# Kernel optimization log

Measured on AMD Instinct MI355X. Metric: run time of the kernel, lower is better.

Reference implementation:

```python
import jax, jax.numpy as jnp
import numpy as np

VOCAB, EMBED, HIDDEN, NCLS = 50257, 1024, 4096, 3
B, S = 4096, 128


def ternary_quant(w):
    # Per-tensor ternary quantization: scale = mean |w|, weights in {-s, 0, +s}.
    s = jnp.mean(jnp.abs(w))
    return jnp.round(jnp.clip(w / s, -1.0, 1.0)) * s


def layer_norm(x, g, b, eps=1e-5):
    mu = jnp.mean(x, axis=-1, keepdims=True)
    var = jnp.mean(jnp.square(x - mu), axis=-1, keepdims=True)
    return (x - mu) * jax.lax.rsqrt(var + eps) * g + b


def setup_inputs() -> dict:
    key = jax.random.key(0)
    ks = jax.random.split(key, 12)
    input_ids = jax.random.randint(ks[0], (B, S), 0, VOCAB, dtype=jnp.int32)
    emb = jax.random.normal(ks[1], (VOCAB, EMBED), dtype=jnp.float32) * 0.02
    emb = emb.at[0].set(0.0)  # padding_idx=0
    w1 = jax.random.normal(ks[2], (HIDDEN, EMBED), dtype=jnp.float32) * 0.02
    b1 = jnp.zeros((HIDDEN,), jnp.float32)
    w2 = jax.random.normal(ks[3], (HIDDEN // 2, HIDDEN), dtype=jnp.float32) * 0.02
    b2 = jnp.zeros((HIDDEN // 2,), jnp.float32)
    w3 = jax.random.normal(ks[4], (NCLS, HIDDEN // 2), dtype=jnp.float32) * 0.02
    b3 = jnp.zeros((NCLS,), jnp.float32)
    g1 = jnp.ones((HIDDEN,), jnp.float32)
    beta1 = jnp.zeros((HIDDEN,), jnp.float32)
    g2 = jnp.ones((HIDDEN // 2,), jnp.float32)
    beta2 = jnp.zeros((HIDDEN // 2,), jnp.float32)
    return dict(input_ids=input_ids, emb=emb, w1=w1, b1=b1, w2=w2, b2=b2,
                w3=w3, b3=b3, g1=g1, beta1=beta1, g2=g2, beta2=beta2)


def reference(input_ids, emb, w1, b1, w2, b2, w3, b3, g1, beta1, g2, beta2):
    x = emb[input_ids]                                   # (B, S, E)
    mask = (input_ids != 0).astype(x.dtype)[..., None]   # (B, S, 1)
    x = jnp.sum(x * mask, axis=1) / jnp.clip(jnp.sum(mask, axis=1), 1.0)  # (B, E)
    h = jax.nn.gelu(layer_norm(x @ ternary_quant(w1).T + b1, g1, beta1), approximate=False)
    h = jax.nn.gelu(layer_norm(h @ ternary_quant(w2).T + b2, g2, beta2), approximate=False)
    logits = h @ ternary_quant(w3).T + b3                # (B, 3)
    return logits
```

## Files before the change

### kernel.cpp

```cpp
#include <hip/hip_runtime.h>
#include <cstdint>
#include <cstddef>


#define GAS __attribute__((address_space(1)))
#define LAS __attribute__((address_space(3)))

typedef __bf16 bf16x8 __attribute__((ext_vector_type(8)));
typedef float  f32x4  __attribute__((ext_vector_type(4)));
typedef unsigned short u16x8 __attribute__((ext_vector_type(8)));

__device__ __forceinline__ unsigned short f2bf(float f) {
    unsigned int u = __float_as_uint(f);
    u += 0x7FFFu + ((u >> 16) & 1u);
    return (unsigned short)(u >> 16);
}
__device__ __forceinline__ float bf2f(unsigned short h) {
    return __uint_as_float(((unsigned int)h) << 16);
}

static constexpr int BB = 4096;
static constexpr int SS = 128;
static constexpr int EE = 1024;
static constexpr int HH = 4096;
static constexpr int H2D = 2048;
static constexpr int VOCAB = 50257;

static constexpr size_t OFF_S    = 0;
static constexpr size_t OFF_X    = 4096;
static constexpr size_t SZ_X     = (size_t)BB * EE * 2;
static constexpr size_t OFF_EMBH = OFF_X + SZ_X;
static constexpr size_t SZ_EMBH  = (size_t)VOCAB * EE * 2;
static constexpr size_t OFF_Q1   = OFF_EMBH;
static constexpr size_t OFF_Q2   = OFF_Q1 + (size_t)HH * EE * 2;
static constexpr size_t OFF_C    = OFF_Q2 + (size_t)H2D * HH * 2;
static constexpr size_t OFF_H1   = OFF_EMBH + SZ_EMBH;
static constexpr size_t OFF_H2   = OFF_Q1;


__global__ void zero_sums(double* s) {
    if (threadIdx.x < 3) s[threadIdx.x] = 0.0;
}

__global__ __launch_bounds__(256) void emb2bf_kernel(const float* __restrict__ e,
                                                     unsigned short* __restrict__ o) {
    const int n8 = (VOCAB * EE) / 8;
    for (int i = blockIdx.x * 256 + threadIdx.x; i < n8; i += gridDim.x * 256) {
        const float4 v0 = ((const float4*)e)[2 * i];
        const float4 v1 = ((const float4*)e)[2 * i + 1];
        union { unsigned short u[8]; uint4 q; } r;
        r.u[0] = f2bf(v0.x); r.u[1] = f2bf(v0.y); r.u[2] = f2bf(v0.z); r.u[3] = f2bf(v0.w);
        r.u[4] = f2bf(v1.x); r.u[5] = f2bf(v1.y); r.u[6] = f2bf(v1.z); r.u[7] = f2bf(v1.w);
        ((uint4*)o)[i] = r.q;
    }
}

__global__ __launch_bounds__(256) void absum_all(const float* __restrict__ w1,
                                                 const float* __restrict__ w2,
                                                 const float* __restrict__ w3,
                                                 double* __restrict__ sums) {
    const int bid = blockIdx.x;
    const float* w; int n; double* out; int b0; int nb;
    if (bid < 1024)      { w = w1; n = HH * EE;  out = sums + 0; b0 = bid;        nb = 1024; }
    else if (bid < 3072) { w = w2; n = H2D * HH; out = sums + 1; b0 = bid - 1024; nb = 2048; }
    else                 { w = w3; n = 3 * H2D;  out = sums + 2; b0 = bid - 3072; nb = 24;   }
    const int tid = threadIdx.x;
    const int lane = tid & 63, wid = tid >> 6;
    double acc = 0.0;
    for (int i = b0 * 256 + tid; i < n; i += nb * 256)
        acc += (double)fabsf(w[i]);
    for (int o = 32; o; o >>= 1) acc += __shfl_down(acc, o);
    __shared__ double r[4];
    if (lane == 0) r[wid] = acc;
    __syncthreads();
    if (tid == 0) atomicAdd(out, r[0] + r[1] + r[2] + r[3]);
}

__global__ __launch_bounds__(256) void quant_all(const float* __restrict__ w1,
                                                 const float* __restrict__ w2,
                                                 const double* __restrict__ sums,
                                                 unsigned short* __restrict__ q1,
                                                 unsigned short* __restrict__ q2) {
    const int bid = blockIdx.x;
    const float* w; int n; unsigned short* q; int b0; int nb; double ssum; double dn;
    if (bid < 4096) { w = w1; n = HH * EE;  q = q1; b0 = bid;        nb = 4096; ssum = sums[0]; dn = (double)(HH) * EE; }
    else            { w = w2; n = H2D * HH; q = q2; b0 = bid - 4096; nb = 8192; ssum = sums[1]; dn = (double)(H2D) * HH; }
    const float inv_s = (float)(dn / ssum);
    for (int i = b0 * 256 + threadIdx.x; i < n; i += nb * 256) {
        float t = w[i] * inv_s;
        t = fminf(1.f, fmaxf(-1.f, t));
        q[i] = f2bf(rintf(t));
    }
}

__global__ __launch_bounds__(256) void pool_kernel(const int* __restrict__ ids,
                                                   const unsigned short* __restrict__ embh,
                                                   unsigned short* __restrict__ X) {
    const int tid  = threadIdx.x;
    const int half = tid >> 7;
    const int t    = tid & 127;
    const int b    = blockIdx.x * 2 + half;
    __shared__ int sid[2 * SS];
    sid[tid] = ids[(size_t)blockIdx.x * 2 * SS + tid];
    __syncthreads();
    const int col  = t * 8;
    const int base = half * SS;
    float a[8] = {};
    int cnt = 0;
    #pragma unroll 8
    for (int s = 0; s < SS; ++s) {
        const int id = sid[base + s];
        cnt += (id != 0);
        const u16x8 v = *(const u16x8*)(embh + (size_t)id * EE + col);
        #pragma unroll
        for (int j = 0; j < 8; ++j) a[j] += bf2f(v[j]);
    }
    const float inv = 1.f / (float)(cnt ? cnt : 1);
    u16x8 o;
    #pragma unroll
    for (int j = 0; j < 8; ++j) o[j] = f2bf(a[j] * inv);
    *(u16x8*)(X + (size_t)b * EE + col) = o;
}

__global__ __launch_bounds__(256) void gemm_bt(const unsigned short* __restrict__ A,
                                               const unsigned short* __restrict__ B,
                                               float* __restrict__ C, int M, int N, int K) {
    __shared__ unsigned short sA[128 * 32];
    __shared__ unsigned short sB[128 * 32];
    const int tid  = threadIdx.x;
    const int wid  = tid >> 6;
    const int lane = tid & 63;
    const int wm = wid >> 1, wn = wid & 1;
    const int quad = lane >> 4;
    const int l16  = lane & 15;
    const int mBase = blockIdx.y * 128;
    const int nBase = blockIdx.x * 128;

    f32x4 acc[4][4] = {};

    const int srow = tid >> 2;
    const int scol = (tid & 3) * 8;
    const size_t aOff0 = (size_t)(mBase + srow) * K + scol;
    const size_t aOff1 = aOff0 + (size_t)64 * K;
    const size_t bOff0 = (size_t)(nBase + srow) * K + scol;
    const size_t bOff1 = bOff0 + (size_t)64 * K;
    unsigned short* ldsA0 = &sA[wid * 512];
    unsigned short* ldsA1 = &sA[2048 + wid * 512];
    unsigned short* ldsB0 = &sB[wid * 512];
    unsigned short* ldsB1 = &sB[2048 + wid * 512];

    for (int k0 = 0; k0 < K; k0 += 32) {
        __syncthreads();
        __builtin_amdgcn_global_load_lds((const GAS void*)(A + aOff0 + k0), (LAS void*)ldsA0, 16, 0, 0);
        __builtin_amdgcn_global_load_lds((const GAS void*)(A + aOff1 + k0), (LAS void*)ldsA1, 16, 0, 0);
        __builtin_amdgcn_global_load_lds((const GAS void*)(B + bOff0 + k0), (LAS void*)ldsB0, 16, 0, 0);
        __builtin_amdgcn_global_load_lds((const GAS void*)(B + bOff1 + k0), (LAS void*)ldsB1, 16, 0, 0);
        __syncthreads();

        bf16x8 af[4], bfr[4];
        #pragma unroll
        for (int i = 0; i < 4; ++i) {
            const int rowA = wm * 64 + i * 16 + l16;
            af[i]  = *(const bf16x8*)(&sA[rowA * 32 + quad * 8]);
            const int rowB = wn * 64 + i * 16 + l16;
            bfr[i] = *(const bf16x8*)(&sB[rowB * 32 + quad * 8]);
        }
        #pragma unroll
        for (int i = 0; i < 4; ++i)
            #pragma unroll
            for (int j = 0; j < 4; ++j)
                acc[i][j] = __builtin_amdgcn_mfma_f32_16x16x32_bf16(af[i], bfr[j], acc[i][j], 0, 0, 0);
    }

    #pragma unroll
    for (int i = 0; i < 4; ++i) {
        const int row0 = mBase + wm * 64 + i * 16 + quad * 4;
        #pragma unroll
        for (int j = 0; j < 4; ++j) {
            const int col = nBase + wn * 64 + j * 16 + l16;
            #pragma unroll
            for (int r = 0; r < 4; ++r)
                C[(size_t)(row0 + r) * N + col] = acc[i][j][r];
        }
    }
}

__global__ __launch_bounds__(256) void ln_gelu_kernel(const float* __restrict__ Cm,
                                                      const double* __restrict__ ssum, double nw,
                                                      const float* __restrict__ bias,
                                                      const float* __restrict__ gamma,
                                                      const float* __restrict__ beta,
                                                      unsigned short* __restrict__ H, int N) {
    __shared__ float buf[4096];
    __shared__ float redS[4], redQ[4];
    const int row = blockIdx.x, tid = threadIdx.x;
    const int lane = tid & 63, wid = tid >> 6;
    const float s = (float)(ssum[0] / nw);
    float ps = 0.f, pq = 0.f;
    for (int c = tid; c < N; c += 256) {
        const float y = Cm[(size_t)row * N + c] * s + bias[c];
        buf[c] = y;
        ps += y; pq += y * y;
    }
    for (int o = 32; o; o >>= 1) { ps += __shfl_down(ps, o); pq += __shfl_down(pq, o); }
    if (lane == 0) { redS[wid] = ps; redQ[wid] = pq; }
    __syncthreads();
    const float sum = redS[0] + redS[1] + redS[2] + redS[3];
    const float sq  = redQ[0] + redQ[1] + redQ[2] + redQ[3];
    const float mu  = sum / (float)N;
    float var = sq / (float)N - mu * mu;
    var = fmaxf(var, 0.f);
    const float inv = rsqrtf(var + 1e-5f);
    for (int c = tid; c < N; c += 256) {
        const float y = (buf[c] - mu) * inv * gamma[c] + beta[c];
        const float g = 0.5f * y * (1.f + erff(y * 0.70710678118654752f));
        H[(size_t)row * N + c] = f2bf(g);
    }
}

__global__ __launch_bounds__(256) void final_kernel(const unsigned short* __restrict__ H2,
                                                    const float* __restrict__ w3,
                                                    const double* __restrict__ ssum,
                                                    const float* __restrict__ b3,
                                                    float* __restrict__ out) {
    const int row = blockIdx.x, tid = threadIdx.x;
    const int lane = tid & 63, wid = tid >> 6;
    const float inv_s3 = (float)((double)(3 * H2D) / ssum[0]);
    float a0 = 0.f, a1 = 0.f, a2 = 0.f;
    for (int k = tid; k < H2D; k += 256) {
        const float h = bf2f(H2[(size_t)row * H2D + k]);
        const float q0 = rintf(fminf(1.f, fmaxf(-1.f, w3[k] * inv_s3)));
        const float q1 = rintf(fminf(1.f, fmaxf(-1.f, w3[H2D + k] * inv_s3)));
        const float q2 = rintf(fminf(1.f, fmaxf(-1.f, w3[2 * H2D + k] * inv_s3)));
        a0 += h * q0; a1 += h * q1; a2 += h * q2;
    }
    for (int o = 32; o; o >>= 1) {
        a0 += __shfl_down(a0, o); a1 += __shfl_down(a1, o); a2 += __shfl_down(a2, o);
    }
    __shared__ float r[3][4];
    if (lane == 0) { r[0][wid] = a0; r[1][wid] = a1; r[2][wid] = a2; }
    __syncthreads();
    if (tid < 3) {
        const float s3 = (float)(ssum[0] / (double)(3 * H2D));
        out[(size_t)row * 3 + tid] =
            (r[tid][0] + r[tid][1] + r[tid][2] + r[tid][3]) * s3 + b3[tid];
    }
}


extern "C" void kernel_launch(void* const* d_in, const int* in_sizes, int n_in,
                              void* d_out, int out_size, void* d_ws, size_t ws_size,
                              hipStream_t stream) {
    const int*   ids = (const int*)d_in[0];
    const float* emb = (const float*)d_in[1];
    const float* w1  = (const float*)d_in[2];
    const float* b1  = (const float*)d_in[3];
    const float* w2  = (const float*)d_in[4];
    const float* b2  = (const float*)d_in[5];
    const float* w3  = (const float*)d_in[6];
    const float* b3  = (const float*)d_in[7];
    const float* g1  = (const float*)d_in[8];
    const float* be1 = (const float*)d_in[9];
    const float* g2  = (const float*)d_in[10];
    const float* be2 = (const float*)d_in[11];
    float* out = (float*)d_out;
    char* ws = (char*)d_ws;

    double*         sums = (double*)(ws + OFF_S);
    unsigned short* X    = (unsigned short*)(ws + OFF_X);
    unsigned short* embh = (unsigned short*)(ws + OFF_EMBH);
    unsigned short* q1   = (unsigned short*)(ws + OFF_Q1);
    unsigned short* q2   = (unsigned short*)(ws + OFF_Q2);
    float*          Cbuf = (float*)(ws + OFF_C);
    unsigned short* H1   = (unsigned short*)(ws + OFF_H1);
    unsigned short* H2   = (unsigned short*)(ws + OFF_H2);

    emb2bf_kernel<<<4096, 256, 0, stream>>>(emb, embh);
    pool_kernel<<<BB / 2, 256, 0, stream>>>(ids, embh, X);

    zero_sums<<<1, 64, 0, stream>>>(sums);
    absum_all<<<3096, 256, 0, stream>>>(w1, w2, w3, sums);
    quant_all<<<12288, 256, 0, stream>>>(w1, w2, sums, q1, q2);

    gemm_bt<<<dim3(HH / 128, BB / 128), 256, 0, stream>>>(X, q1, Cbuf, BB, HH, EE);
    ln_gelu_kernel<<<BB, 256, 0, stream>>>(Cbuf, sums + 0, (double)HH * (double)EE,
                                           b1, g1, be1, H1, HH);
    gemm_bt<<<dim3(H2D / 128, BB / 128), 256, 0, stream>>>(H1, q2, Cbuf, BB, H2D, HH);
    ln_gelu_kernel<<<BB, 256, 0, stream>>>(Cbuf, sums + 1, (double)H2D * (double)HH,
                                           b2, g2, be2, H2, H2D);
    final_kernel<<<BB, 256, 0, stream>>>(H2, w3, sums + 2, b3, out);
}
```

Measured before the change: 771.7 us.

## Fuse embedding conversion with weight abs-sum and sort pooled ids by page

Merges the embedding fp32-to-bf16 conversion and the ternary abs-sum reduction into one launch, so the two independent memory-bound passes share a single grid and one launch is removed. The pooling kernel now counting-sorts each row's token ids by 1024-row bucket before gathering, aiming for more local embedding reads, and counts nonzero ids with a shared atomic. The sort adds shared-memory atomics and several barriers per block. Floating-point summation order changes slightly.

```diff
diff --git a/kernel.cpp b/kernel.cpp
--- a/kernel.cpp
+++ b/kernel.cpp
@@ -42,34 +42,35 @@
     if (threadIdx.x < 3) s[threadIdx.x] = 0.0;
 }
 
-__global__ __launch_bounds__(256) void emb2bf_kernel(const float* __restrict__ e,
-                                                     unsigned short* __restrict__ o) {
-    const int n8 = (VOCAB * EE) / 8;
-    for (int i = blockIdx.x * 256 + threadIdx.x; i < n8; i += gridDim.x * 256) {
-        const float4 v0 = ((const float4*)e)[2 * i];
-        const float4 v1 = ((const float4*)e)[2 * i + 1];
-        union { unsigned short u[8]; uint4 q; } r;
-        r.u[0] = f2bf(v0.x); r.u[1] = f2bf(v0.y); r.u[2] = f2bf(v0.z); r.u[3] = f2bf(v0.w);
-        r.u[4] = f2bf(v1.x); r.u[5] = f2bf(v1.y); r.u[6] = f2bf(v1.z); r.u[7] = f2bf(v1.w);
-        ((uint4*)o)[i] = r.q;
-    }
-}
-
-__global__ __launch_bounds__(256) void absum_all(const float* __restrict__ w1,
-                                                 const float* __restrict__ w2,
-                                                 const float* __restrict__ w3,
-                                                 double* __restrict__ sums) {
+__global__ __launch_bounds__(256) void prep_kernel(const float* __restrict__ e,
+                                                   unsigned short* __restrict__ o,
+                                                   const float* __restrict__ w1,
+                                                   const float* __restrict__ w2,
+                                                   const float* __restrict__ w3,
+                                                   double* __restrict__ sums) {
     const int bid = blockIdx.x;
+    const int tid = threadIdx.x;
+    if (bid < 4096) {
+        const int n8 = (VOCAB * EE) / 8;
+        for (int i = bid * 256 + tid; i < n8; i += 4096 * 256) {
+            const float4 v0 = ((const float4*)e)[2 * i];
+            const float4 v1 = ((const float4*)e)[2 * i + 1];
+            union { unsigned short u[8]; uint4 q; } r;
+            r.u[0] = f2bf(v0.x); r.u[1] = f2bf(v0.y); r.u[2] = f2bf(v0.z); r.u[3] = f2bf(v0.w);
+            r.u[4] = f2bf(v1.x); r.u[5] = f2bf(v1.y); r.u[6] = f2bf(v1.z); r.u[7] = f2bf(v1.w);
+            ((uint4*)o)[i] = r.q;
+        }
+        return;
+    }
     const float* w; int n; double* out; int b0; int nb;
-    if (bid < 1024)      { w = w1; n = HH * EE;  out = sums + 0; b0 = bid;        nb = 1024; }
-    else if (bid < 3072) { w = w2; n = H2D * HH; out = sums + 1; b0 = bid - 1024; nb = 2048; }
-    else                 { w = w3; n = 3 * H2D;  out = sums + 2; b0 = bid - 3072; nb = 24;   }
-    const int tid = threadIdx.x;
+    if (bid < 5120)      { w = w1; n = HH * EE;  out = sums + 0; b0 = bid - 4096; nb = 1024; }
+    else if (bid < 7168) { w = w2; n = H2D * HH; out = sums + 1; b0 = bid - 5120; nb = 2048; }
+    else                 { w = w3; n = 3 * H2D;  out = sums + 2; b0 = bid - 7168; nb = 24;   }
     const int lane = tid & 63, wid = tid >> 6;
     double acc = 0.0;
     for (int i = b0 * 256 + tid; i < n; i += nb * 256)
         acc += (double)fabsf(w[i]);
-    for (int o = 32; o; o >>= 1) acc += __shfl_down(acc, o);
+    for (int off = 32; off; off >>= 1) acc += __shfl_down(acc, off);
     __shared__ double r[4];
     if (lane == 0) r[wid] = acc;
     __syncthreads();
@@ -96,30 +97,49 @@
 __global__ __launch_bounds__(256) void pool_kernel(const int* __restrict__ ids,
                                                    const unsigned short* __restrict__ embh,
                                                    unsigned short* __restrict__ X) {
-    const int tid  = threadIdx.x;
-    const int half = tid >> 7;
-    const int t    = tid & 127;
-    const int b    = blockIdx.x * 2 + half;
-    __shared__ int sid[2 * SS];
-    sid[tid] = ids[(size_t)blockIdx.x * 2 * SS + tid];
-    __syncthreads();
-    const int col  = t * 8;
-    const int base = half * SS;
+    const int tid = threadIdx.x;
+    const int row = tid >> 7;
+    const int t   = tid & 127;
+    __shared__ int sid[256];
+    __shared__ int sorted_ids[2][128];
+    __shared__ int cnt[2][64];
+    __shared__ int pos[2][64];
+    __shared__ int nz[2];
+    sid[tid] = ids[(size_t)blockIdx.x * 256 + tid];
+    if (tid < 128) ((int*)cnt)[tid] = 0;
+    if (tid < 2) nz[tid] = 0;
+    __syncthreads();
+    const int myid = sid[tid];
+    const int ph = myid >> 10;
+    atomicAdd(&cnt[row][ph], 1);
+    if (myid != 0) atomicAdd(&nz[row], 1);
+    __syncthreads();
+    if (tid < 2) {
+        int s = 0;
+        #pragma unroll
+        for (int p = 0; p < 64; ++p) { pos[tid][p] = s; s += cnt[tid][p]; }
+    }
+    __syncthreads();
+    const int where = atomicAdd(&pos[row][ph], 1);
+    sorted_ids[row][where] = myid;
+    __syncthreads();
+
+    const int col = t * 8;
     float a[8] = {};
-    int cnt = 0;
     #pragma unroll 8
-    for (int s = 0; s < SS; ++s) {
-        const int id = sid[base + s];
-        cnt += (id != 0);
+    for (int s = 0; s < 128; ++s) {
+        const int id = sorted_ids[row][s];
         const u16x8 v = *(const u16x8*)(embh + (size_t)id * EE + col);
         #pragma unroll
         for (int j = 0; j < 8; ++j) a[j] += bf2f(v[j]);
     }
-    const float inv = 1.f / (float)(cnt ? cnt : 1);
-    u16x8 o;
+    const int c = nz[row];
+    const float inv = 1.f / (float)(c ? c : 1);
+    u16x8 ov;
     #pragma unroll
-    for (int j = 0; j < 8; ++j) o[j] = f2bf(a[j] * inv);
-    *(u16x8*)(X + (size_t)b * EE + col) = o;
+    for (int j = 0; j < 8; ++j) ov[j] = f2bf(a[j] * inv);
+    const int b = blockIdx.x * 2 + row;
+    *(u16x8*)(X + (size_t)b * EE + col) = ov;
 }
 
 __global__ __launch_bounds__(256) void gemm_bt(const unsigned short* __restrict__ A,
@@ -275,11 +295,10 @@
     unsigned short* H1   = (unsigned short*)(ws + OFF_H1);
     unsigned short* H2   = (unsigned short*)(ws + OFF_H2);
 
-    emb2bf_kernel<<<4096, 256, 0, stream>>>(emb, embh);
+    zero_sums<<<1, 64, 0, stream>>>(sums);
+    prep_kernel<<<7192, 256, 0, stream>>>(emb, embh, w1, w2, w3, sums);
     pool_kernel<<<BB / 2, 256, 0, stream>>>(ids, embh, X);
 
-    zero_sums<<<1, 64, 0, stream>>>(sums);
-    absum_all<<<3096, 256, 0, stream>>>(w1, w2, w3, sums);
     quant_all<<<12288, 256, 0, stream>>>(w1, w2, sums, q1, q2);
 
     gemm_bt<<<dim3(HH / 128, BB / 128), 256, 0, stream>>>(X, q1, Cbuf, BB, HH, EE);
```

New measurement: 723.0 us. 1.07x faster.
